# Kernel tuning notes

Hardware: AMD Instinct MI355X
Metric: run time of the kernel (lower is better)

## Reference

```python
import jax, jax.numpy as jnp
import numpy as np

B, T, K = 8192, 256, 16
N_TRANS = 4  # 0: s2u, 1: u2s_n0, 2: u2s_n1_d2, 3: u2s_n1_dgt2  (DistanceCRF)


def setup_inputs() -> dict:
    key = jax.random.key(0)
    ks = jax.random.split(key, 8)
    emissions = jax.random.normal(ks[0], (B, T, K), dtype=jnp.float32)
    tags = jax.random.randint(ks[1], (B, T), 0, K, dtype=jnp.int32)
    who2who = jax.random.randint(ks[2], (B, T - 1), 0, 2, dtype=jnp.int32)
    init_count = jax.random.randint(ks[3], (B, T - 1), 0, 2, dtype=jnp.int32)
    distance = jax.random.randint(ks[4], (B, T - 1), 0, 2, dtype=jnp.int32)
    class_weights = jax.random.uniform(ks[5], (K,), dtype=jnp.float32, minval=0.5, maxval=2.0)
    trans_stack = jax.random.normal(ks[6], (N_TRANS, K, K), dtype=jnp.float32) * 0.1
    start_scores = jax.random.normal(ks[7], (K,), dtype=jnp.float32) * 0.1
    return {
        'emissions': emissions, 'tags': tags, 'who2who': who2who,
        'init_count': init_count, 'distance': distance,
        'class_weights': class_weights, 'trans_stack': trans_stack,
        'start_scores': start_scores,
    }


def _trans_index(who2who, init_count, distance):
    # Mirrors MultiTurnCRF._get_trans for variant='DistanceCRF':
    #   w==1 -> s2u; w==0 & init_count==0 -> u2s_n0;
    #   w==0 & init>0 & distance==0 -> u2s_n1_d2; else u2s_n1_dgt2
    return jnp.where(who2who == 1, 0,
           jnp.where(init_count == 0, 1,
           jnp.where(distance == 0, 2, 3)))


def _crf_seq(em, tags, tidx, class_weights, trans_stack, start_scores):
    # em: [T, K], tags: [T], tidx: [T-1]
    w = class_weights[tags]                               # [T]
    em_gold = jnp.take_along_axis(em, tags[:, None], axis=1)[:, 0]   # [T]
    tr_gold = trans_stack[tidx, tags[:-1], tags[1:]]      # [T-1]
    gold = w[0] * (start_scores[tags[0]] + em_gold[0]) \
           + jnp.sum(w[1:] * (tr_gold + em_gold[1:]))

    def step(alpha, xs):
        ti, e = xs
        tr = trans_stack[ti]                              # [K, K]
        alpha = jax.nn.logsumexp(alpha[:, None] + tr + e[None, :], axis=0)
        return alpha, None

    alpha0 = start_scores + em[0]
    alphaT, _ = jax.lax.scan(step, alpha0, (tidx, em[1:]))
    log_Z = jax.nn.logsumexp(alphaT)
    return gold, log_Z


def reference(emissions, tags, who2who, init_count, distance,
              class_weights, trans_stack, start_scores):
    tidx = _trans_index(who2who, init_count, distance)    # [B, T-1]
    gold, log_Z = jax.vmap(_crf_seq, in_axes=(0, 0, 0, None, None, None))(
        emissions, tags, tidx, class_weights, trans_stack, start_scores)
    return gold, log_Z
```

## Files before the change

kernel.cpp:

```cpp
#include <hip/hip_runtime.h>

#define T_LEN 256
#define K 16
#define B_TOT 8192
#define RSCALE 3.2734375f
#define L2E    1.44269504f

typedef __attribute__((ext_vector_type(8))) short bf16x8;
typedef __attribute__((ext_vector_type(4))) float f32x4;
typedef __attribute__((ext_vector_type(4))) int   i32x4;

union FRAG { i32x4 i; bf16x8 b; };

__device__ __forceinline__ unsigned pkbf(float hi, float lo) {
    return __builtin_amdgcn_perm(__float_as_uint(hi), __float_as_uint(lo), 0x07060302u);
}

__global__ __launch_bounds__(256) void pack_ctrl(
    const int* __restrict__ tags, const int* __restrict__ w2w,
    const int* __restrict__ ic,   const int* __restrict__ ds,
    const float* __restrict__ cw, const float* __restrict__ trans,
    const float* __restrict__ start, const float* __restrict__ em,
    unsigned char* __restrict__ tidxB, float* __restrict__ goldp)
{
    int idx = blockIdx.x * 256 + threadIdx.x;
    int b = idx >> 8, t = idx & 255;
    int tag = tags[idx];
    float emg = em[(size_t)idx * 16 + tag];
    unsigned char ti = 0;
    float g;
    if (t == 0) {
        g = cw[tag] * (start[tag] + emg);
    } else {
        int off = b * (T_LEN - 1) + (t - 1);
        int tidx = (w2w[off] == 1) ? 0 : ((ic[off] == 0) ? 1 : ((ds[off] == 0) ? 2 : 3));
        ti = (unsigned char)tidx;
        int tp = tags[idx - 1];
        g = cw[tag] * (trans[tidx * 256 + tp * 16 + tag] + emg);
    }
    tidxB[idx] = ti;
    goldp[idx] = g;
}

__global__ __launch_bounds__(256) void gold_red(
    const float* __restrict__ goldp, float* __restrict__ out)
{
    int b = blockIdx.x * 4 + (threadIdx.x >> 6);
    int l = threadIdx.x & 63;
    const float* p = goldp + (size_t)b * 256;
    float s = (p[l] + p[l + 64]) + (p[l + 128] + p[l + 192]);
#pragma unroll
    for (int m = 1; m < 64; m <<= 1) s += __shfl_xor(s, m, 64);
    if (l == 0) out[b] = s;
}

__global__ __launch_bounds__(64) void crf_fwd(
    const float* __restrict__ em, const float* __restrict__ trans,
    const float* __restrict__ start, const unsigned char* __restrict__ tidxB,
    float* __restrict__ out)
{
    const int lane = threadIdx.x;
    const int s = lane & 15;
    const int g = lane >> 4;
    const int b = blockIdx.x * 16 + s;

    FRAG A[4];
#pragma unroll
    for (int c = 0; c < 4; ++c) {
        float x[4], xl[4];
#pragma unroll
        for (int e = 0; e < 4; ++e) {
            float v = __expf(trans[c * 256 + (4 * g + e) * 16 + s]);
            x[e] = v;
            xl[e] = v - __uint_as_float(__float_as_uint(v) & 0xFFFF0000u);
        }
        A[c].i = (i32x4){ (int)pkbf(x[1], x[0]),  (int)pkbf(x[3], x[2]),
                          (int)pkbf(xl[1], xl[0]), (int)pkbf(xl[3], xl[2]) };
    }

    const float* emb = em + (size_t)b * 4096 + g * 4;
    const unsigned char* tb = tidxB + (size_t)b * 256;

    f32x4 emq[4];
#pragma unroll
    for (int t = 0; t < 4; ++t) emq[t] = *(const f32x4*)(emb + t * 16);

    unsigned vp0, vp1;
    {
        f32x4 st4 = *(const f32x4*)(start + 4 * g);
        float v0 = __expf(st4[0] + emq[0][0]);
        float v1 = __expf(st4[1] + emq[0][1]);
        float v2 = __expf(st4[2] + emq[0][2]);
        float v3 = __expf(st4[3] + emq[0][3]);
        vp0 = pkbf(v1, v0); vp1 = pkbf(v3, v2);
    }

    f32x4 exq[2];
    {
        f32x4 e1 = emq[1], r;
#pragma unroll
        for (int i = 0; i < 4; ++i) r[i] = __builtin_exp2f(fmaf(e1[i], L2E, -RSCALE * L2E));
        exq[1] = r;
    }

    float logC = 0.0f;
    uint4 tq  = *(const uint4*)(tb);
    uint4 tqn = *(const uint4*)(tb + 16);

    auto STEP = [&](int t, int k) __attribute__((always_inline)) {
        unsigned dw = (k < 4) ? tq.x : (k < 8) ? tq.y : (k < 12) ? tq.z : tq.w;
        int ti = (int)((dw >> ((k & 3) * 8)) & 0xFFu);

        int p0 = (int)vp0, p1 = (int)vp1;
        int m00 = (ti == 0) ? p0 : 0, m01 = (ti == 0) ? p1 : 0;
        int m10 = (ti == 1) ? p0 : 0, m11 = (ti == 1) ? p1 : 0;
        int m20 = (ti == 2) ? p0 : 0, m21 = (ti == 2) ? p1 : 0;
        int m30 = (ti == 3) ? p0 : 0, m31 = (ti == 3) ? p1 : 0;
        FRAG B0, B1, B2, B3;
        B0.i = (i32x4){m00, m01, m00, m01};
        B1.i = (i32x4){m10, m11, m10, m11};
        B2.i = (i32x4){m20, m21, m20, m21};
        B3.i = (i32x4){m30, m31, m30, m31};

        f32x4 za = __builtin_amdgcn_mfma_f32_16x16x32_bf16(A[0].b, B0.b, (f32x4)(0.0f), 0, 0, 0);
        za       = __builtin_amdgcn_mfma_f32_16x16x32_bf16(A[1].b, B1.b, za,            0, 0, 0);
        f32x4 zb = __builtin_amdgcn_mfma_f32_16x16x32_bf16(A[2].b, B2.b, (f32x4)(0.0f), 0, 0, 0);
        zb       = __builtin_amdgcn_mfma_f32_16x16x32_bf16(A[3].b, B3.b, zb,            0, 0, 0);

        f32x4 d = (za + zb) * exq[k & 1];

        int tt = t + 4; if (tt > 255) tt = 255;
        emq[k & 3] = *(const f32x4*)(emb + (size_t)tt * 16);

        {
            f32x4 en = emq[(k + 1) & 3], r;
#pragma unroll
            for (int i = 0; i < 4; ++i) r[i] = __builtin_exp2f(fmaf(en[i], L2E, -RSCALE * L2E));
            exq[(k + 1) & 1] = r;
        }

        if (k == 15) {
            float mx = fmaxf(fmaxf(d[0], d[1]), fmaxf(d[2], d[3]));
            mx = fmaxf(mx, __shfl_xor(mx, 16, 64));
            mx = fmaxf(mx, __shfl_xor(mx, 32, 64));
            int e2; (void)frexpf(mx, &e2);
            d[0] = ldexpf(d[0], -e2); d[1] = ldexpf(d[1], -e2);
            d[2] = ldexpf(d[2], -e2); d[3] = ldexpf(d[3], -e2);
            logC += (float)e2 * 0.69314718f;
        }

        vp0 = pkbf(d[1], d[0]);
        vp1 = pkbf(d[3], d[2]);
    };

#pragma unroll
    for (int k = 1; k < 16; ++k) STEP(k, k);
    for (int blk = 1; blk < 16; ++blk) {
        tq = tqn;
        int nb = (blk + 1 < 16) ? blk + 1 : 15;
        tqn = *(const uint4*)(tb + nb * 16);
#pragma unroll
        for (int k = 0; k < 16; ++k) STEP(blk * 16 + k, k);
    }

    float f0 = __uint_as_float(vp0 << 16);
    float f1 = __uint_as_float(vp0 & 0xFFFF0000u);
    float f2 = __uint_as_float(vp1 << 16);
    float f3 = __uint_as_float(vp1 & 0xFFFF0000u);
    float su = (f0 + f1) + (f2 + f3);
    su += __shfl_xor(su, 16, 64);
    su += __shfl_xor(su, 32, 64);
    if (g == 0) out[B_TOT + b] = logf(su) + 255.0f * RSCALE + logC;
}

extern "C" void kernel_launch(void* const* d_in, const int* in_sizes, int n_in,
                              void* d_out, int out_size, void* d_ws, size_t ws_size,
                              hipStream_t stream) {
    const float* emissions     = (const float*)d_in[0];
    const int*   tags          = (const int*)  d_in[1];
    const int*   who2who       = (const int*)  d_in[2];
    const int*   init_count    = (const int*)  d_in[3];
    const int*   distance      = (const int*)  d_in[4];
    const float* class_weights = (const float*)d_in[5];
    const float* trans_stack   = (const float*)d_in[6];
    const float* start_scores  = (const float*)d_in[7];
    float* out = (float*)d_out;

    unsigned char* tidxB = (unsigned char*)d_ws;
    float*         goldp = (float*)((char*)d_ws + B_TOT * T_LEN);

    hipLaunchKernelGGL(pack_ctrl, dim3(B_TOT), dim3(256), 0, stream,
                       tags, who2who, init_count, distance,
                       class_weights, trans_stack, start_scores, emissions,
                       tidxB, goldp);

    hipLaunchKernelGGL(crf_fwd, dim3(B_TOT / 16), dim3(64), 0, stream,
                       emissions, trans_stack, start_scores, tidxB, out);

    hipLaunchKernelGGL(gold_red, dim3(B_TOT / 4), dim3(256), 0, stream,
                       goldp, out);
}
```

Baseline: 280.7 us.

## Split CRF forward scan into vector prefix and parallel matrix-product suffix

The sequential forward recursion is split in two. The first 192 steps run as a vector scan (crf_vec), and the last 64 steps run as a 16x16 matrix product per sequence in a separate kernel (crf_mat) with one wave per batch. A combine kernel multiplies the two results and folds in the gold-score reduction. The gold emission gather moves into the scan kernels, and the tag and transition index are packed into one control byte. pkbf now rounds instead of truncating. The aim is to shorten the serial critical path and add parallelism, at the cost of extra launches, workspace traffic for the 16x16 matrices, and a different bf16 rounding.

```diff
diff --git a/kernel.cpp b/kernel.cpp
--- a/kernel.cpp
+++ b/kernel.cpp
@@ -5,6 +5,9 @@
 #define B_TOT 8192
 #define RSCALE 3.2734375f
 #define L2E    1.44269504f
+#define VT     192
+#define NBLKV  12
+#define MT     64
 
 typedef __attribute__((ext_vector_type(8))) short bf16x8;
 typedef __attribute__((ext_vector_type(4))) float f32x4;
@@ -13,51 +16,40 @@
 union FRAG { i32x4 i; bf16x8 b; };
 
 __device__ __forceinline__ unsigned pkbf(float hi, float lo) {
-    return __builtin_amdgcn_perm(__float_as_uint(hi), __float_as_uint(lo), 0x07060302u);
+    unsigned uh = __float_as_uint(hi) + 0x8000u;
+    unsigned ul = __float_as_uint(lo) + 0x8000u;
+    return __builtin_amdgcn_perm(uh, ul, 0x07060302u);
 }
 
 __global__ __launch_bounds__(256) void pack_ctrl(
     const int* __restrict__ tags, const int* __restrict__ w2w,
     const int* __restrict__ ic,   const int* __restrict__ ds,
     const float* __restrict__ cw, const float* __restrict__ trans,
-    const float* __restrict__ start, const float* __restrict__ em,
-    unsigned char* __restrict__ tidxB, float* __restrict__ goldp)
+    const float* __restrict__ start,
+    unsigned char* __restrict__ ctrl, float* __restrict__ goldp)
 {
     int idx = blockIdx.x * 256 + threadIdx.x;
     int b = idx >> 8, t = idx & 255;
     int tag = tags[idx];
-    float emg = em[(size_t)idx * 16 + tag];
-    unsigned char ti = 0;
+    unsigned char byte = (unsigned char)tag;
     float g;
     if (t == 0) {
-        g = cw[tag] * (start[tag] + emg);
+        g = cw[tag] * start[tag];
     } else {
         int off = b * (T_LEN - 1) + (t - 1);
         int tidx = (w2w[off] == 1) ? 0 : ((ic[off] == 0) ? 1 : ((ds[off] == 0) ? 2 : 3));
-        ti = (unsigned char)tidx;
-        int tp = tags[idx - 1];
-        g = cw[tag] * (trans[tidx * 256 + tp * 16 + tag] + emg);
-    }
-    tidxB[idx] = ti;
+        byte |= (unsigned char)(tidx << 4);
+        g = cw[tag] * trans[tidx * 256 + tags[idx - 1] * 16 + tag];
+    }
+    ctrl[idx]  = byte;
     goldp[idx] = g;
 }
 
-__global__ __launch_bounds__(256) void gold_red(
-    const float* __restrict__ goldp, float* __restrict__ out)
-{
-    int b = blockIdx.x * 4 + (threadIdx.x >> 6);
-    int l = threadIdx.x & 63;
-    const float* p = goldp + (size_t)b * 256;
-    float s = (p[l] + p[l + 64]) + (p[l + 128] + p[l + 192]);
-#pragma unroll
-    for (int m = 1; m < 64; m <<= 1) s += __shfl_xor(s, m, 64);
-    if (l == 0) out[b] = s;
-}
-
-__global__ __launch_bounds__(64) void crf_fwd(
+__global__ __launch_bounds__(64) void crf_vec(
     const float* __restrict__ em, const float* __restrict__ trans,
-    const float* __restrict__ start, const unsigned char* __restrict__ tidxB,
-    float* __restrict__ out)
+    const float* __restrict__ start, const float* __restrict__ cw,
+    const unsigned char* __restrict__ ctrl,
+    float* __restrict__ amid, float* __restrict__ logCv, float* __restrict__ emgv)
 {
     const int lane = threadIdx.x;
     const int s = lane & 15;
@@ -79,37 +71,47 @@
     }
 
     const float* emb = em + (size_t)b * 4096 + g * 4;
-    const unsigned char* tb = tidxB + (size_t)b * 256;
-
-    f32x4 emq[4];
-#pragma unroll
-    for (int t = 0; t < 4; ++t) emq[t] = *(const f32x4*)(emb + t * 16);
+    const unsigned char* tb = ctrl + (size_t)b * 256;
+    const f32x4 cwq = *(const f32x4*)(cw + 4 * g);
+
+    f32x4 emq[8];
+#pragma unroll
+    for (int t = 0; t < 8; ++t) emq[t] = *(const f32x4*)(emb + t * 16);
+
+    uint4 tq  = *(const uint4*)(tb);
+    uint4 tqn = *(const uint4*)(tb + 16);
 
     unsigned vp0, vp1;
+    f32x4 dcur;
+    float ge = 0.0f, logC = 0.0f;
+    f32x4 exq[2];
+
     {
+        int tag0 = (int)(tq.x & 15u);
         f32x4 st4 = *(const f32x4*)(start + 4 * g);
-        float v0 = __expf(st4[0] + emq[0][0]);
-        float v1 = __expf(st4[1] + emq[0][1]);
-        float v2 = __expf(st4[2] + emq[0][2]);
-        float v3 = __expf(st4[3] + emq[0][3]);
-        vp0 = pkbf(v1, v0); vp1 = pkbf(v3, v2);
-    }
-
-    f32x4 exq[2];
-    {
+        f32x4 q = emq[0];
+        dcur[0] = __expf(st4[0] + q[0]); dcur[1] = __expf(st4[1] + q[1]);
+        dcur[2] = __expf(st4[2] + q[2]); dcur[3] = __expf(st4[3] + q[3]);
+        vp0 = pkbf(dcur[1], dcur[0]); vp1 = pkbf(dcur[3], dcur[2]);
+        float e01 = (tag0 & 1) ? q[1] : q[0];
+        float e23 = (tag0 & 1) ? q[3] : q[2];
+        float esel = (tag0 & 2) ? e23 : e01;
+        float c01 = (tag0 & 1) ? cwq[1] : cwq[0];
+        float c23 = (tag0 & 1) ? cwq[3] : cwq[2];
+        float csel = (tag0 & 2) ? c23 : c01;
+        ge = (g == (tag0 >> 2)) ? csel * esel : 0.0f;
         f32x4 e1 = emq[1], r;
 #pragma unroll
         for (int i = 0; i < 4; ++i) r[i] = __builtin_exp2f(fmaf(e1[i], L2E, -RSCALE * L2E));
         exq[1] = r;
-    }
-
-    float logC = 0.0f;
-    uint4 tq  = *(const uint4*)(tb);
-    uint4 tqn = *(const uint4*)(tb + 16);
+        emq[0] = *(const f32x4*)(emb + 8 * 16);
+    }
 
     auto STEP = [&](int t, int k) __attribute__((always_inline)) {
         unsigned dw = (k < 4) ? tq.x : (k < 8) ? tq.y : (k < 12) ? tq.z : tq.w;
-        int ti = (int)((dw >> ((k & 3) * 8)) & 0xFFu);
+        unsigned byte = (dw >> ((k & 3) * 8)) & 0xFFu;
+        int tag = (int)(byte & 15u);
+        int ti  = (int)(byte >> 4);
 
         int p0 = (int)vp0, p1 = (int)vp1;
         int m00 = (ti == 0) ? p0 : 0, m01 = (ti == 0) ? p1 : 0;
@@ -122,22 +124,28 @@
         B2.i = (i32x4){m20, m21, m20, m21};
         B3.i = (i32x4){m30, m31, m30, m31};
 
-        f32x4 za = __builtin_amdgcn_mfma_f32_16x16x32_bf16(A[0].b, B0.b, (f32x4)(0.0f), 0, 0, 0);
-        za       = __builtin_amdgcn_mfma_f32_16x16x32_bf16(A[1].b, B1.b, za,            0, 0, 0);
-        f32x4 zb = __builtin_amdgcn_mfma_f32_16x16x32_bf16(A[2].b, B2.b, (f32x4)(0.0f), 0, 0, 0);
-        zb       = __builtin_amdgcn_mfma_f32_16x16x32_bf16(A[3].b, B3.b, zb,            0, 0, 0);
-
-        f32x4 d = (za + zb) * exq[k & 1];
-
-        int tt = t + 4; if (tt > 255) tt = 255;
-        emq[k & 3] = *(const f32x4*)(emb + (size_t)tt * 16);
+        f32x4 z0 = __builtin_amdgcn_mfma_f32_16x16x32_bf16(A[0].b, B0.b, (f32x4)(0.0f), 0, 0, 0);
+        f32x4 z1 = __builtin_amdgcn_mfma_f32_16x16x32_bf16(A[1].b, B1.b, (f32x4)(0.0f), 0, 0, 0);
+        f32x4 z2 = __builtin_amdgcn_mfma_f32_16x16x32_bf16(A[2].b, B2.b, (f32x4)(0.0f), 0, 0, 0);
+        f32x4 z3 = __builtin_amdgcn_mfma_f32_16x16x32_bf16(A[3].b, B3.b, (f32x4)(0.0f), 0, 0, 0);
+        f32x4 d = ((z0 + z1) + (z2 + z3)) * exq[k & 1];
+
+        f32x4 q = emq[k & 7];
+        float e01 = (tag & 1) ? q[1] : q[0];
+        float e23 = (tag & 1) ? q[3] : q[2];
+        float esel = (tag & 2) ? e23 : e01;
+        float c01 = (tag & 1) ? cwq[1] : cwq[0];
+        float c23 = (tag & 1) ? cwq[3] : cwq[2];
+        float csel = (tag & 2) ? c23 : c01;
+        if (g == (tag >> 2)) ge = fmaf(csel, esel, ge);
 
         {
-            f32x4 en = emq[(k + 1) & 3], r;
+            f32x4 en = emq[(k + 1) & 7], r;
 #pragma unroll
             for (int i = 0; i < 4; ++i) r[i] = __builtin_exp2f(fmaf(en[i], L2E, -RSCALE * L2E));
             exq[(k + 1) & 1] = r;
         }
+        emq[k & 7] = *(const f32x4*)(emb + (size_t)(t + 8) * 16);
 
         if (k == 15) {
             float mx = fmaxf(fmaxf(d[0], d[1]), fmaxf(d[2], d[3]));
@@ -148,29 +156,181 @@
             d[2] = ldexpf(d[2], -e2); d[3] = ldexpf(d[3], -e2);
             logC += (float)e2 * 0.69314718f;
         }
-
+        dcur = d;
         vp0 = pkbf(d[1], d[0]);
         vp1 = pkbf(d[3], d[2]);
     };
 
 #pragma unroll
     for (int k = 1; k < 16; ++k) STEP(k, k);
-    for (int blk = 1; blk < 16; ++blk) {
+    for (int blk = 1; blk < NBLKV; ++blk) {
         tq = tqn;
-        int nb = (blk + 1 < 16) ? blk + 1 : 15;
+        int nb = (blk + 1 < NBLKV) ? blk + 1 : NBLKV - 1;
         tqn = *(const uint4*)(tb + nb * 16);
 #pragma unroll
         for (int k = 0; k < 16; ++k) STEP(blk * 16 + k, k);
     }
 
-    float f0 = __uint_as_float(vp0 << 16);
-    float f1 = __uint_as_float(vp0 & 0xFFFF0000u);
-    float f2 = __uint_as_float(vp1 << 16);
-    float f3 = __uint_as_float(vp1 & 0xFFFF0000u);
-    float su = (f0 + f1) + (f2 + f3);
-    su += __shfl_xor(su, 16, 64);
-    su += __shfl_xor(su, 32, 64);
-    if (g == 0) out[B_TOT + b] = logf(su) + 255.0f * RSCALE + logC;
+#pragma unroll
+    for (int i = 0; i < 4; ++i) amid[b * 16 + 4 * g + i] = dcur[i];
+    ge += __shfl_xor(ge, 16, 64);
+    ge += __shfl_xor(ge, 32, 64);
+    if (g == 0) { logCv[b] = logC; emgv[b] = ge; }
+}
+
+__global__ __launch_bounds__(256) void crf_mat(
+    const float* __restrict__ em, const float* __restrict__ trans,
+    const float* __restrict__ cw, const unsigned char* __restrict__ ctrl,
+    float* __restrict__ Mout, float* __restrict__ logCm, float* __restrict__ emgm)
+{
+    const int lane = threadIdx.x & 63;
+    const int wv   = threadIdx.x >> 6;
+    const int s = lane & 15;
+    const int g = lane >> 4;
+    const int b = blockIdx.x * 4 + wv;
+
+    FRAG A[4];
+#pragma unroll
+    for (int c = 0; c < 4; ++c) {
+        float x[4], xl[4];
+#pragma unroll
+        for (int e = 0; e < 4; ++e) {
+            float v = __expf(trans[c * 256 + (4 * g + e) * 16 + s]);
+            x[e] = v;
+            xl[e] = v - __uint_as_float(__float_as_uint(v) & 0xFFFF0000u);
+        }
+        A[c].i = (i32x4){ (int)pkbf(x[1], x[0]),  (int)pkbf(x[3], x[2]),
+                          (int)pkbf(xl[1], xl[0]), (int)pkbf(xl[3], xl[2]) };
+    }
+
+    const float* emb = em + (size_t)b * 4096 + g * 4;
+    const unsigned char* tb = ctrl + (size_t)b * 256 + VT;
+    const f32x4 cwq = *(const f32x4*)(cw + 4 * g);
+
+    f32x4 emq[4];
+#pragma unroll
+    for (int j = 0; j < 4; ++j) emq[j] = *(const f32x4*)(emb + (size_t)(VT + j) * 16);
+
+    f32x4 dcur;
+    unsigned vp0, vp1;
+    {
+        dcur[0] = (4 * g + 0 == s) ? 1.0f : 0.0f;
+        dcur[1] = (4 * g + 1 == s) ? 1.0f : 0.0f;
+        dcur[2] = (4 * g + 2 == s) ? 1.0f : 0.0f;
+        dcur[3] = (4 * g + 3 == s) ? 1.0f : 0.0f;
+        vp0 = pkbf(dcur[1], dcur[0]); vp1 = pkbf(dcur[3], dcur[2]);
+    }
+
+    f32x4 exq[2];
+    {
+        f32x4 e0 = emq[0], r;
+#pragma unroll
+        for (int i = 0; i < 4; ++i) r[i] = __builtin_exp2f(fmaf(e0[i], L2E, -RSCALE * L2E));
+        exq[0] = r;
+    }
+
+    float ge = 0.0f, logC = 0.0f;
+    uint4 tq  = *(const uint4*)(tb);
+    uint4 tqn = *(const uint4*)(tb + 16);
+
+    auto STEP = [&](int kk, int k) __attribute__((always_inline)) {
+        int t = VT + kk;
+        unsigned dw = (k < 4) ? tq.x : (k < 8) ? tq.y : (k < 12) ? tq.z : tq.w;
+        unsigned byte = (dw >> ((k & 3) * 8)) & 0xFFu;
+        int tagu = __builtin_amdgcn_readfirstlane((int)(byte & 15u));
+        int tiu  = __builtin_amdgcn_readfirstlane((int)(byte >> 4));
+
+        FRAG B; B.i = (i32x4){(int)vp0, (int)vp1, (int)vp0, (int)vp1};
+        f32x4 z;
+        if (tiu == 0)      z = __builtin_amdgcn_mfma_f32_16x16x32_bf16(A[0].b, B.b, (f32x4)(0.0f), 0, 0, 0);
+        else if (tiu == 1) z = __builtin_amdgcn_mfma_f32_16x16x32_bf16(A[1].b, B.b, (f32x4)(0.0f), 0, 0, 0);
+        else if (tiu == 2) z = __builtin_amdgcn_mfma_f32_16x16x32_bf16(A[2].b, B.b, (f32x4)(0.0f), 0, 0, 0);
+        else               z = __builtin_amdgcn_mfma_f32_16x16x32_bf16(A[3].b, B.b, (f32x4)(0.0f), 0, 0, 0);
+        f32x4 d = z * exq[k & 1];
+
+        f32x4 q = emq[k & 3];
+        float e01 = (tagu & 1) ? q[1] : q[0];
+        float e23 = (tagu & 1) ? q[3] : q[2];
+        float esel = (tagu & 2) ? e23 : e01;
+        float c01 = (tagu & 1) ? cwq[1] : cwq[0];
+        float c23 = (tagu & 1) ? cwq[3] : cwq[2];
+        float csel = (tagu & 2) ? c23 : c01;
+        if (s == 0 && g == (tagu >> 2)) ge = fmaf(csel, esel, ge);
+
+        {
+            f32x4 en = emq[(k + 1) & 3], r;
+#pragma unroll
+            for (int i = 0; i < 4; ++i) r[i] = __builtin_exp2f(fmaf(en[i], L2E, -RSCALE * L2E));
+            exq[(k + 1) & 1] = r;
+        }
+        int tt = t + 4; if (tt > 255) tt = 255;
+        emq[k & 3] = *(const f32x4*)(emb + (size_t)tt * 16);
+
+        if (k == 15) {
+            float mx = fmaxf(fmaxf(d[0], d[1]), fmaxf(d[2], d[3]));
+#pragma unroll
+            for (int m = 1; m < 64; m <<= 1) mx = fmaxf(mx, __shfl_xor(mx, m, 64));
+            int e2; (void)frexpf(mx, &e2);
+            d[0] = ldexpf(d[0], -e2); d[1] = ldexpf(d[1], -e2);
+            d[2] = ldexpf(d[2], -e2); d[3] = ldexpf(d[3], -e2);
+            logC += (float)e2 * 0.69314718f;
+        }
+        dcur = d;
+        vp0 = pkbf(d[1], d[0]);
+        vp1 = pkbf(d[3], d[2]);
+    };
+
+#pragma unroll
+    for (int k = 0; k < 16; ++k) STEP(k, k);
+    for (int blk = 1; blk < 4; ++blk) {
+        tq = tqn;
+        int nb = (blk + 1 < 4) ? blk + 1 : 3;
+        tqn = *(const uint4*)(tb + nb * 16);
+#pragma unroll
+        for (int k = 0; k < 16; ++k) STEP(blk * 16 + k, k);
+    }
+
+#pragma unroll
+    for (int i = 0; i < 4; ++i) Mout[(size_t)b * 256 + (4 * g + i) * 16 + s] = dcur[i];
+    ge += __shfl_xor(ge, 16, 64);
+    ge += __shfl_xor(ge, 32, 64);
+    if (lane == 0) { logCm[b] = logC; emgm[b] = ge; }
+}
+
+__global__ __launch_bounds__(256) void combine(
+    const float* __restrict__ Mout, const float* __restrict__ amid,
+    const float* __restrict__ goldp, const float* __restrict__ emgv,
+    const float* __restrict__ emgm,  const float* __restrict__ logCv,
+    const float* __restrict__ logCm, float* __restrict__ out)
+{
+    const int lane = threadIdx.x & 63;
+    const int wv   = threadIdx.x >> 6;
+    const int q = lane >> 4, r = lane & 15;
+    const int b = blockIdx.x * 16 + wv * 4 + q;
+
+    const float4* Mr = (const float4*)(Mout + (size_t)b * 256 + r * 16);
+    const float4* av = (const float4*)(amid + (size_t)b * 16);
+    float4 m0 = Mr[0], m1 = Mr[1], m2 = Mr[2], m3 = Mr[3];
+    float4 a0 = av[0], a1 = av[1], a2 = av[2], a3 = av[3];
+    float at = m0.x * a0.x + m0.y * a0.y + m0.z * a0.z + m0.w * a0.w
+             + m1.x * a1.x + m1.y * a1.y + m1.z * a1.z + m1.w * a1.w
+             + m2.x * a2.x + m2.y * a2.y + m2.z * a2.z + m2.w * a2.w
+             + m3.x * a3.x + m3.y * a3.y + m3.z * a3.z + m3.w * a3.w;
+
+    const float4* gp = (const float4*)(goldp + (size_t)b * 256 + r * 16);
+    float4 g0 = gp[0], g1 = gp[1], g2 = gp[2], g3 = gp[3];
+    float gs = (g0.x + g0.y + g0.z + g0.w) + (g1.x + g1.y + g1.z + g1.w)
+             + (g2.x + g2.y + g2.z + g2.w) + (g3.x + g3.y + g3.z + g3.w);
+
+#pragma unroll
+    for (int m = 1; m < 16; m <<= 1) {
+        at += __shfl_xor(at, m, 64);
+        gs += __shfl_xor(gs, m, 64);
+    }
+    if (r == 0) {
+        out[b]         = gs + emgv[b] + emgm[b];
+        out[B_TOT + b] = logf(at) + logCv[b] + logCm[b] + 255.0f * RSCALE;
+    }
 }
 
 extern "C" void kernel_launch(void* const* d_in, const int* in_sizes, int n_in,
@@ -186,17 +346,28 @@
     const float* start_scores  = (const float*)d_in[7];
     float* out = (float*)d_out;
 
-    unsigned char* tidxB = (unsigned char*)d_ws;
-    float*         goldp = (float*)((char*)d_ws + B_TOT * T_LEN);
+    char* ws = (char*)d_ws;
+    unsigned char* ctrl  = (unsigned char*)ws;
+    float* goldp = (float*)(ws + (2 << 20));
+    float* Mout  = (float*)(ws + (10 << 20));
+    float* amid  = (float*)(ws + (18 << 20));
+    float* logCv = (float*)(ws + (19 << 20));
+    float* logCm = (float*)(ws + (19 << 20) + (64 << 10));
+    float* emgv  = (float*)(ws + (19 << 20) + (128 << 10));
+    float* emgm  = (float*)(ws + (19 << 20) + (192 << 10));
 
     hipLaunchKernelGGL(pack_ctrl, dim3(B_TOT), dim3(256), 0, stream,
                        tags, who2who, init_count, distance,
-                       class_weights, trans_stack, start_scores, emissions,
-                       tidxB, goldp);
-
-    hipLaunchKernelGGL(crf_fwd, dim3(B_TOT / 16), dim3(64), 0, stream,
-                       emissions, trans_stack, start_scores, tidxB, out);
-
-    hipLaunchKernelGGL(gold_red, dim3(B_TOT / 4), dim3(256), 0, stream,
-                       goldp, out);
-}
+                       class_weights, trans_stack, start_scores, ctrl, goldp);
+
+    hipLaunchKernelGGL(crf_vec, dim3(B_TOT / 16), dim3(64), 0, stream,
+                       emissions, trans_stack, start_scores, class_weights,
+                       ctrl, amid, logCv, emgv);
+
+    hipLaunchKernelGGL(crf_mat, dim3(B_TOT / 4), dim3(256), 0, stream,
+                       emissions, trans_stack, class_weights, ctrl,
+                       Mout, logCm, emgm);
+
+    hipLaunchKernelGGL(combine, dim3(B_TOT / 16), dim3(256), 0, stream,
+                       Mout, amid, goldp, emgv, emgm, logCv, logCm, out);
+}
```

Result: slower. 292.9 us (+4.3%).
